# Optimization experiments

Hardware: AMD Instinct MI355X
Metric: run time of the kernel (lower is better)

The kernel has to match this reference:

```python
import jax, jax.numpy as jnp
import numpy as np

B, S, HID, NH, K = 4, 1500, 1024, 16, 64
DH = HID // NH  # 64


def _rel_bias(pos_emb, length):
    # pos_emb: [2K+1, d]; Shaw-style relative position embedding lookup -> [S, S, d]
    kk = (pos_emb.shape[0] - 1) // 2
    idx = jnp.arange(length)
    dist = jnp.clip(idx[None, :] - idx[:, None], -kk, kk) + kk
    return pos_emb[dist]


def setup_inputs() -> dict:
    key = jax.random.key(0)
    ks = jax.random.split(key, 12)
    sq = 1.0 / np.sqrt(HID)
    inp = {
        "query": jax.random.normal(ks[0], (B, S, HID), jnp.float32),
        "key": jax.random.normal(ks[1], (B, S, HID), jnp.float32),
        "value": jax.random.normal(ks[2], (B, S, HID), jnp.float32),
        # per-head QKV projections stacked over heads: [NH, HID, DH]
        "Wq": jax.random.normal(ks[3], (NH, HID, DH), jnp.float32) * sq,
        "bq": jnp.zeros((NH, DH), jnp.float32),
        "Wk": jax.random.normal(ks[4], (NH, HID, DH), jnp.float32) * sq,
        "bk": jnp.zeros((NH, DH), jnp.float32),
        "Wv": jax.random.normal(ks[5], (NH, HID, DH), jnp.float32) * sq,
        "bv": jnp.zeros((NH, DH), jnp.float32),
        # relative position tables [2K+1, DH]
        "pos_k": jax.random.normal(ks[6], (2 * K + 1, DH), jnp.float32) * 0.1,
        "pos_v": jax.random.normal(ks[7], (2 * K + 1, DH), jnp.float32) * 0.1,
        # output projection
        "W_fc": jax.random.normal(ks[8], (HID, HID), jnp.float32) * sq,
        "b_fc": jnp.zeros((HID,), jnp.float32),
    }
    return inp


def reference(query, key, value, Wq, bq, Wk, bk, Wv, bv, pos_k, pos_v, W_fc, b_fc):
    seq = query.shape[1]
    k_bias = _rel_bias(pos_k, seq)  # [S, S, DH]
    v_bias = _rel_bias(pos_v, seq)  # [S, S, DH]

    # batched per-head projections: [B, NH, S, DH]
    q = jnp.einsum('bsh,nhd->bnsd', query, Wq) + bq[None, :, None, :]
    k = jnp.einsum('bsh,nhd->bnsd', key, Wk) + bk[None, :, None, :]
    v = jnp.einsum('bsh,nhd->bnsd', value, Wv) + bv[None, :, None, :]

    attn_1 = jnp.einsum('bnqd,bnkd->bnqk', q, k)
    attn_2 = jnp.einsum('bnqd,qkd->bnqk', q, k_bias)  # Shaw relative key bias
    scores = (attn_1 + attn_2) / jnp.sqrt(jnp.float32(DH))
    w = jax.nn.softmax(scores, axis=-1)  # [B, NH, S, S]

    values_1 = jnp.einsum('bnqk,bnkd->bnqd', w, v)
    values_2 = jnp.einsum('bnqk,qkd->bnqd', w, v_bias)  # Shaw relative value bias
    heads = values_1 + values_2  # [B, NH, S, DH]

    # concat heads in head order -> [B, S, HID]
    hidden = jnp.transpose(heads, (0, 2, 1, 3)).reshape(query.shape[0], seq, -1)
    return hidden @ W_fc + b_fc
```

## Files before the change

kernel.cpp:

```cpp
#include <hip/hip_runtime.h>
#include <stdint.h>

typedef unsigned short u16;
typedef __attribute__((ext_vector_type(8))) short bf16x8;
typedef __attribute__((ext_vector_type(4))) float f32x4;

#define MFMA16(a, b, c) __builtin_amdgcn_mfma_f32_16x16x32_bf16(a, b, c, 0, 0, 0)

__device__ __forceinline__ u16 f2bf(float x) {
  union { float f; uint32_t u; } v; v.f = x;
  uint32_t r = (v.u + 0x7FFFu + ((v.u >> 16) & 1u)) >> 16;
  return (u16)r;
}
__device__ __forceinline__ float bf2f(u16 h) {
  union { uint32_t u; float f; } v; v.u = ((uint32_t)h) << 16; return v.f;
}
__device__ __forceinline__ uint cvt_pk_bf16(float a, float b) {
  uint r;
  asm("v_cvt_pk_bf16_f32 %0, %1, %2" : "=v"(r) : "v"(a), "v"(b));
  return r;
}
__device__ __forceinline__ void gll16(const void* g, void* s) {
  __builtin_amdgcn_global_load_lds((const __attribute__((address_space(1))) unsigned int*)g,
                                   (__attribute__((address_space(3))) unsigned int*)s, 16, 0, 0);
}


__global__ __launch_bounds__(256) void pack_x_kernel(const float* __restrict__ q,
                                                     const float* __restrict__ k,
                                                     const float* __restrict__ v,
                                                     u16* __restrict__ X) {
  const float* src = blockIdx.z == 0 ? q : (blockIdx.z == 1 ? k : v);
  u16* dst = X + (size_t)blockIdx.z * (6016UL * 1024UL);
  size_t idx = (size_t)blockIdx.x * 1024 + (size_t)threadIdx.x * 4;
  float4 f = *(const float4*)(src + idx);
  uint2 o;
  o.x = cvt_pk_bf16(f.x, f.y);
  o.y = cvt_pk_bf16(f.z, f.w);
  *(uint2*)(dst + idx) = o;
}

__global__ __launch_bounds__(256) void pack_w_kernel(const float* __restrict__ Wq,
                                                     const float* __restrict__ Wk,
                                                     const float* __restrict__ Wv,
                                                     const float* __restrict__ Wfc,
                                                     const float* __restrict__ bq,
                                                     const float* __restrict__ bk,
                                                     const float* __restrict__ bv,
                                                     const float* __restrict__ posk,
                                                     const float* __restrict__ posv,
                                                     u16* __restrict__ Wt,
                                                     u16* __restrict__ Wfct,
                                                     float* __restrict__ biascat,
                                                     u16* __restrict__ poskbf,
                                                     u16* __restrict__ posvT) {
  __shared__ float tile[64][65];
  const int bi = blockIdx.x;
  if (bi == 1024) {
    for (int i = threadIdx.x; i < 1024; i += 256) {
      biascat[i] = bq[i]; biascat[1024 + i] = bk[i]; biascat[2048 + i] = bv[i];
    }
    for (int i = threadIdx.x; i < 144 * 64; i += 256) {
      int r = i >> 6;
      poskbf[i] = (r < 129) ? f2bf(posk[i]) : (u16)0;
    }
    const int d = threadIdx.x & 63, rr = threadIdx.x >> 6;
#pragma unroll
    for (int j = 0; j < 34; ++j) {
      const int r = rr * 34 + j;
      posvT[d * 136 + r] = (r < 129) ? f2bf(posv[(size_t)r * 64 + d]) : (u16)0;
    }
    return;
  }
  const int r = threadIdx.x >> 2, c0 = (threadIdx.x & 3) * 16;
  const float* src;
  u16* outp;
  if (bi < 768) {
    const int z = bi >> 8, rem = bi & 255, n = rem >> 4, h0 = (rem & 15) * 64;
    const float* W = z == 0 ? Wq : (z == 1 ? Wk : Wv);
    src = W + (size_t)n * 65536 + (size_t)(h0 + r) * 64 + c0;
    outp = Wt + (size_t)z * (1024UL * 1024UL) + (size_t)(n * 64 + r) * 1024 + h0 + c0;
  } else {
    const int t = bi - 768;
    const int i0 = (t & 15) * 64, o0 = (t >> 4) * 64;
    src = Wfc + (size_t)(i0 + r) * 1024 + o0 + c0;
    outp = Wfct + (size_t)(o0 + r) * 1024 + i0 + c0;
  }
#pragma unroll
  for (int j = 0; j < 16; j += 4) {
    float4 f = *(const float4*)(src + j);
    tile[r][c0 + j] = f.x; tile[r][c0 + j + 1] = f.y;
    tile[r][c0 + j + 2] = f.z; tile[r][c0 + j + 3] = f.w;
  }
  __syncthreads();
#pragma unroll
  for (int j = 0; j < 16; ++j) outp[j] = f2bf(tile[c0 + j][r]);
}

__global__ __launch_bounds__(256) void vtrans_kernel(const u16* __restrict__ qkv,
                                                     u16* __restrict__ Vt) {
  const size_t ZS = 4UL * 16 * 1536 * 64;
  __shared__ u16 t[64][72];
  const int bh = blockIdx.x & 63, s0 = (blockIdx.x >> 6) * 64;
  const u16* src = qkv + 2 * ZS + (size_t)bh * (1536UL * 64UL) + (size_t)s0 * 64;
  const int r = threadIdx.x >> 2, c0 = (threadIdx.x & 3) * 16;
  *(uint4*)&t[r][c0]     = *(const uint4*)(src + (size_t)r * 64 + c0);
  *(uint4*)&t[r][c0 + 8] = *(const uint4*)(src + (size_t)r * 64 + c0 + 8);
  __syncthreads();
  uint4 a, bvec;
  uint tmp[8];
#pragma unroll
  for (int j = 0; j < 8; ++j)
    tmp[j] = (uint)t[c0 + 2 * j][r] | ((uint)t[c0 + 2 * j + 1][r] << 16);
  a.x = tmp[0]; a.y = tmp[1]; a.z = tmp[2]; a.w = tmp[3];
  bvec.x = tmp[4]; bvec.y = tmp[5]; bvec.z = tmp[6]; bvec.w = tmp[7];
  u16* dst = Vt + (size_t)(bh * 64 + r) * 1536 + s0 + c0;
  *(uint4*)dst = a;
  *(uint4*)(dst + 8) = bvec;
}

__global__ __launch_bounds__(256, 4) void gemm_bt_kernel(
    const u16* __restrict__ Abase, long aStride,
    const u16* __restrict__ Bbase, long bStride,
    const float* __restrict__ biasBase, long biasStride,
    u16* __restrict__ outBF, float* __restrict__ outF, int mode) {
  __shared__ u16 As[2][128 * 32];
  __shared__ u16 Bs[2][128 * 32];

  const int nwg = 376 * gridDim.z;
  const int cpx = nwg >> 3;
  const int lid = blockIdx.x + (blockIdx.y << 3) + blockIdx.z * 376;
  const int swz = (lid & 7) * cpx + (lid >> 3);
  const int z = swz / 376;
  const int rem = swz - z * 376;
  const int m0 = (rem >> 3) * 128, n0 = (rem & 7) * 128;

  const u16* A = Abase + (size_t)z * aStride;
  const u16* Bt = Bbase + (size_t)z * bStride;
  const float* bias = biasBase + (size_t)z * biasStride;
  const int tid = threadIdx.x, w = tid >> 6, lane = tid & 63;
  const int quad = lane >> 4, l16 = lane & 15;
  const int wm = w >> 1, wn = w & 1;
  const int srow = w * 16 + (lane >> 2);
  const int scol = (lane & 3) * 8;
  const u16* gA = A + (size_t)(m0 + srow) * 1024 + scol;
  const u16* gB = Bt + (size_t)(n0 + srow) * 1024 + scol;
  const int lo0 = (w * 16) * 32;
  const int lo1 = (64 + w * 16) * 32;

  f32x4 acc[4][4];
  const f32x4 zf = {0.f, 0.f, 0.f, 0.f};
#pragma unroll
  for (int a = 0; a < 4; ++a)
#pragma unroll
    for (int b = 0; b < 4; ++b) acc[a][b] = zf;

  auto stage = [&](int buf) {
    gll16(gA, &As[buf][lo0]);
    gll16(gA + 64 * 1024, &As[buf][lo1]);
    gll16(gB, &Bs[buf][lo0]);
    gll16(gB + 64 * 1024, &Bs[buf][lo1]);
    gA += 32; gB += 32;
  };
  auto compute = [&](int buf) {
    bf16x8 af[4], bfr[4];
#pragma unroll
    for (int f = 0; f < 4; ++f) {
      af[f]  = *(const bf16x8*)(&As[buf][(wm * 64 + f * 16 + l16) * 32 + quad * 8]);
      bfr[f] = *(const bf16x8*)(&Bs[buf][(wn * 64 + f * 16 + l16) * 32 + quad * 8]);
    }
#pragma unroll
    for (int fm = 0; fm < 4; ++fm)
#pragma unroll
      for (int fn = 0; fn < 4; ++fn)
        acc[fm][fn] = MFMA16(af[fm], bfr[fn], acc[fm][fn]);
  };

  stage(0);

#define GEMM_WAIT_BAR() do {                                  \
    asm volatile("s_waitcnt vmcnt(0)" ::: "memory");          \
    __builtin_amdgcn_sched_barrier(0);                        \
    __builtin_amdgcn_s_barrier();                             \
    __builtin_amdgcn_sched_barrier(0);                        \
  } while (0)

#pragma unroll 1
  for (int pr = 0; pr < 16; ++pr) {
    GEMM_WAIT_BAR();
    stage(1);
    compute(0);
    GEMM_WAIT_BAR();
    if (pr < 15) stage(0);
    compute(1);
  }
#undef GEMM_WAIT_BAR

  if (mode == 0) {
    const float scale = (z == 0) ? 0.125f : 1.0f;
    u16* out = outBF + (size_t)z * (4UL * 16 * 1536 * 64);
#pragma unroll
    for (int fm = 0; fm < 4; ++fm) {
#pragma unroll
      for (int i = 0; i < 4; ++i) {
        const int m = m0 + wm * 64 + fm * 16 + quad * 4 + i;
        if (m >= 6000) continue;
        const int bb = m / 1500;
        const int s = m - bb * 1500;
#pragma unroll
        for (int fn = 0; fn < 4; ++fn) {
          const int n = n0 + wn * 64 + fn * 16 + l16;
          const float vv = (acc[fm][fn][i] + bias[n]) * scale;
          const int h = n >> 6, d = n & 63;
          out[((size_t)(bb * 16 + h) * 1536 + s) * 64 + d] = f2bf(vv);
        }
      }
    }
  } else {
#pragma unroll
    for (int fm = 0; fm < 4; ++fm) {
#pragma unroll
      for (int i = 0; i < 4; ++i) {
        const int m = m0 + wm * 64 + fm * 16 + quad * 4 + i;
        if (m >= 6000) continue;
#pragma unroll
        for (int fn = 0; fn < 4; ++fn) {
          const int n = n0 + wn * 64 + fn * 16 + l16;
          outF[(size_t)m * 1024 + n] = acc[fm][fn][i] + bias[n];
        }
      }
    }
  }
}

__global__ __launch_bounds__(256, 4) void attn_kernel(const u16* __restrict__ qkv,
                                                      const u16* __restrict__ Vt,
                                                      const u16* __restrict__ poskbf,
                                                      const u16* __restrict__ posvT,
                                                      const float* __restrict__ posv,
                                                      u16* __restrict__ hidden) {
  const size_t ZS = 4UL * 16 * 1536 * 64;
  __shared__ u16 qb_s[64 * 136];
  __shared__ u16 kbuf[2][2048];
  __shared__ u16 vbuf[2][2048];

  const int tid = threadIdx.x;
  const int w = tid >> 6, lane = tid & 63, quad = lane >> 4, l16 = lane & 15;
  const int bi = blockIdx.x;
  const int bh = bi & 63;
  const int q0 = (bi >> 6) * 64, qw0 = q0 + w * 16;
  const int b = bh >> 4;
  const size_t sb = (size_t)bh * (1536UL * 64UL);
  const u16* Qp = qkv + sb;
  const u16* Kp = qkv + ZS + sb;
  const u16* Vtb = Vt + (size_t)bh * (64UL * 1536UL);
  u16* qb_row = qb_s + (w * 16 + l16) * 136;

  const int r8 = lane >> 3, c8 = lane & 7;
  const int vr = lane >> 2, vc = lane & 3;
  const int kprow = ((( (w * 8 + r8) & 15) >> 2) * 8) + (((w * 8 + r8) >> 4) * 4) + ((w * 8 + r8) & 3);
  const u16* kSrc = Kp + (size_t)kprow * 64 + ((c8 ^ r8) * 8);
  const u16* vSrc = Vtb + (size_t)(w * 16 + vr) * 1536 + ((vc ^ ((vr >> 1) & 3)) * 8);
  u16* const kDst = &kbuf[0][0] + w * 512;
  u16* const vDst = &vbuf[0][0] + w * 512;

  gll16(kSrc, kDst);
  gll16(vSrc, vDst);

  const u16* qptr = Qp + (size_t)(qw0 + l16) * 64 + quad * 8;
  const bf16x8 qB0 = *(const bf16x8*)qptr;
  const bf16x8 qB1 = *(const bf16x8*)(qptr + 32);

  const f32x4 zf = {0.f, 0.f, 0.f, 0.f};
#pragma unroll
  for (int nf = 0; nf < 9; ++nf) {
    const u16* bp = poskbf + (size_t)(nf * 16 + l16) * 64 + quad * 8;
    bf16x8 b0 = *(const bf16x8*)bp;
    bf16x8 b1 = *(const bf16x8*)(bp + 32);
    f32x4 c = zf;
    c = MFMA16(qB0, b0, c);
    c = MFMA16(qB1, b1, c);
    const int col = nf * 16 + l16;
    if (col < 136) {
#pragma unroll
      for (int i = 0; i < 4; ++i)
        qb_s[(w * 16 + quad * 4 + i) * 136 + col] = f2bf(c[i]);
    }
  }
  __syncthreads();

  const float L2E = 1.44269504f;
  const float M8 = -8.0f * L2E;
  const float eLow  = __builtin_fmaf(bf2f(qb_row[0]), L2E, M8);
  const float eHigh = __builtin_fmaf(bf2f(qb_row[128]), L2E, M8);

  f32x4 accf[4];
#pragma unroll
  for (int dc = 0; dc < 4; ++dc) accf[dc] = zf;
  float sSimple = 0.f, sLowSave = 0.f, sDall = 0.f, sD0 = 0.f, sD128 = 0.f;

  const int itLowEnd = (qw0 >= 95) ? (((qw0 - 95) >> 5) + 1) : 0;
  const int itHigh0 = (qw0 + 110) >> 5;
  const int dEnd = itHigh0 < 46 ? itHigh0 : 46;

  const int kswz = (quad ^ (l16 & 7)) * 8;
  const int kswz4 = ((quad + 4) ^ (l16 & 7)) * 8;
  const int vpos = (quad ^ ((l16 >> 1) & 3)) * 8;

  const u16* kS = kSrc + 2048;
  const u16* vS = vSrc + 32;

  auto body = [&](int it, const u16* kb, const u16* vbse, bool doStage, int stageOff) {
    if (doStage) {
      gll16(kS, kDst + stageOff);
      gll16(vS, vDst + stageOff);
      kS += 2048; vS += 32;
    }

    if (it == itLowEnd) sLowSave = sSimple;
    const int phase = (it < itLowEnd) ? 0 : ((it >= 46) ? 1 : ((it < dEnd) ? 1 : 2));

    bf16x8 ka00 = *(const bf16x8*)(kb + l16 * 64 + kswz);
    bf16x8 ka01 = *(const bf16x8*)(kb + l16 * 64 + kswz4);
    bf16x8 ka10 = *(const bf16x8*)(kb + (16 + l16) * 64 + kswz);
    bf16x8 ka11 = *(const bf16x8*)(kb + (16 + l16) * 64 + kswz4);
    bf16x8 vb0 = *(const bf16x8*)(vbse + l16 * 32 + vpos);
    bf16x8 vb1 = *(const bf16x8*)(vbse + (16 + l16) * 32 + vpos);
    bf16x8 vb2 = *(const bf16x8*)(vbse + (32 + l16) * 32 + vpos);
    bf16x8 vb3 = *(const bf16x8*)(vbse + (48 + l16) * 32 + vpos);

    float qb[2][4];
    if (phase == 1) {
      const int base = it * 32 + 64 - qw0 - l16 + quad * 8;
#pragma unroll
      for (int cg = 0; cg < 2; ++cg) {
#pragma unroll
        for (int i = 0; i < 4; ++i) {
          int delta = base + cg * 4 + i;
          delta = delta < 0 ? 0 : (delta > 128 ? 128 : delta);
          qb[cg][i] = bf2f(qb_row[delta]);
        }
      }
    }

    f32x4 cc[2];
    cc[0] = zf; cc[1] = zf;
    cc[0] = MFMA16(ka00, qB0, cc[0]);
    cc[0] = MFMA16(ka01, qB1, cc[0]);
    cc[1] = MFMA16(ka10, qB0, cc[1]);
    cc[1] = MFMA16(ka11, qB1, cc[1]);

    float pvv[2][4];
    if (phase != 1) {
      const float eB = (phase == 0) ? eLow : eHigh;
#pragma unroll
      for (int cg = 0; cg < 2; ++cg) {
#pragma unroll
        for (int i = 0; i < 4; ++i) {
          float p = __builtin_amdgcn_exp2f(__builtin_fmaf(cc[cg][i], L2E, eB));
          sSimple += p; pvv[cg][i] = p;
        }
      }
    } else {
      const int kc0 = it * 32;
#pragma unroll
      for (int cg = 0; cg < 2; ++cg) {
        const int krow0 = kc0 + quad * 8 + cg * 4;
        const int dbase = krow0 + 64 - qw0 - l16;
#pragma unroll
        for (int i = 0; i < 4; ++i) {
          int delta = dbase + i;
          delta = delta < 0 ? 0 : (delta > 128 ? 128 : delta);
          const float t = cc[cg][i] + qb[cg][i];
          float p = __builtin_amdgcn_exp2f(__builtin_fmaf(t, L2E, M8));
          if (krow0 + i >= 1500) p = 0.f;
          sDall += p;
          sD0   += (delta == 0)   ? p : 0.f;
          sD128 += (delta == 128) ? p : 0.f;
          pvv[cg][i] = p;
        }
        const uint pk01 = cvt_pk_bf16(pvv[cg][0], pvv[cg][1]);
        const uint pk23 = cvt_pk_bf16(pvv[cg][2], pvv[cg][3]);
        const u16 hb[4] = {(u16)pk01, (u16)(pk01 >> 16), (u16)pk23, (u16)(pk23 >> 16)};
#pragma unroll
        for (int i = 0; i < 4; ++i) {
          int delta = dbase + i;
          delta = delta < 0 ? 0 : (delta > 128 ? 128 : delta);
          if ((delta != 0) & (delta != 128)) qb_row[delta] = hb[i];
        }
      }
    }

    union { uint u[4]; bf16x8 v; } pa;
    pa.u[0] = cvt_pk_bf16(pvv[0][0], pvv[0][1]);
    pa.u[1] = cvt_pk_bf16(pvv[0][2], pvv[0][3]);
    pa.u[2] = cvt_pk_bf16(pvv[1][0], pvv[1][1]);
    pa.u[3] = cvt_pk_bf16(pvv[1][2], pvv[1][3]);

    accf[0] = MFMA16(pa.v, vb0, accf[0]);
    accf[1] = MFMA16(pa.v, vb1, accf[1]);
    accf[2] = MFMA16(pa.v, vb2, accf[2]);
    accf[3] = MFMA16(pa.v, vb3, accf[3]);

    __syncthreads();
  };

#pragma unroll 1
  for (int pr = 0; pr < 23; ++pr) {
    const int it0 = pr * 2;
    body(it0,     &kbuf[0][0], &vbuf[0][0], true, 2048);
    body(it0 + 1, &kbuf[1][0], &vbuf[1][0], true, 0);
  }
  body(46, &kbuf[0][0], &vbuf[0][0], false, 0);

  const float sLow = sLowSave;
  const float sHigh = sSimple - sLowSave;
  float lpart = sSimple + sDall;
  float clow = sLow + sD0;
  float chigh = sHigh + sD128;
#pragma unroll
  for (int m = 16; m <= 32; m <<= 1) {
    lpart += __shfl_xor(lpart, m);
    clow  += __shfl_xor(clow, m);
    chigh += __shfl_xor(chigh, m);
  }
  const float linv = 1.0f / lpart;

  {
    const int qg_row = qw0 + l16;
    if (quad == 0) qb_row[0] = 0;
    const int lim = 64 - qg_row;
    for (int d = 1 + quad; d < lim; d += 4) qb_row[d] = 0;
    const int dlo = 1564 - qg_row;
    for (int d = dlo + quad; d <= 127; d += 4) qb_row[d] = 0;
  }

  f32x4 o2[4];
#pragma unroll
  for (int dc = 0; dc < 4; ++dc) o2[dc] = zf;
#pragma unroll
  for (int kk = 0; kk < 4; ++kk) {
    bf16x8 pa2 = *(const bf16x8*)(qb_row + kk * 32 + quad * 8);
#pragma unroll
    for (int dc = 0; dc < 4; ++dc) {
      bf16x8 vb2r = *(const bf16x8*)(posvT + (size_t)(dc * 16 + l16) * 136 + kk * 32 + quad * 8);
      o2[dc] = MFMA16(pa2, vb2r, o2[dc]);
    }
  }

  float li[4], cl[4], ch[4];
#pragma unroll
  for (int i = 0; i < 4; ++i) {
    const int srcl = quad * 4 + i;
    li[i] = __shfl(linv, srcl);
    cl[i] = __shfl(clow, srcl);
    ch[i] = __shfl(chigh, srcl);
  }

#pragma unroll
  for (int dc = 0; dc < 4; ++dc) {
    const int d = dc * 16 + l16;
    const float pv0 = posv[d], pv1 = posv[128 * 64 + d];
#pragma unroll
    for (int i = 0; i < 4; ++i) {
      const int qg = qw0 + quad * 4 + i;
      if (qg < 1500) {
        const float val = (accf[dc][i] + o2[dc][i] + cl[i] * pv0 + ch[i] * pv1) * li[i];
        hidden[((size_t)(b * 1500 + qg)) * 1024 + (bh & 15) * 64 + d] = f2bf(val);
      }
    }
  }
}

extern "C" void kernel_launch(void* const* d_in, const int* in_sizes, int n_in,
                              void* d_out, int out_size, void* d_ws, size_t ws_size,
                              hipStream_t stream) {
  const float* query = (const float*)d_in[0];
  const float* key   = (const float*)d_in[1];
  const float* value = (const float*)d_in[2];
  const float* Wq = (const float*)d_in[3];
  const float* bq = (const float*)d_in[4];
  const float* Wk = (const float*)d_in[5];
  const float* bk = (const float*)d_in[6];
  const float* Wv = (const float*)d_in[7];
  const float* bv = (const float*)d_in[8];
  const float* posk = (const float*)d_in[9];
  const float* posv = (const float*)d_in[10];
  const float* Wfc = (const float*)d_in[11];
  const float* bfc = (const float*)d_in[12];
  float* out = (float*)d_out;

  char* p = (char*)d_ws;
  u16* X = (u16*)p;        p += 3UL * 6016 * 1024 * 2;
  u16* Wt = (u16*)p;       p += 3UL * 1024 * 1024 * 2;
  u16* Wfct = (u16*)p;     p += 1024UL * 1024 * 2;
  u16* poskbf = (u16*)p;   p += 144UL * 64 * 2;
  u16* posvT = (u16*)p;    p += 64UL * 136 * 2;
  float* biascat = (float*)p; p += 3UL * 1024 * 4;
  u16* qkv = (u16*)p;      p += 3UL * 4 * 16 * 1536 * 64 * 2;
  u16* hidden = X;
  u16* Vt = X + 6291456;

  pack_x_kernel<<<dim3(6000, 1, 3), 256, 0, stream>>>(query, key, value, X);
  pack_w_kernel<<<dim3(1025), 256, 0, stream>>>(Wq, Wk, Wv, Wfc, bq, bk, bv, posk, posv,
                                                Wt, Wfct, biascat, poskbf, posvT);

  gemm_bt_kernel<<<dim3(8, 47, 3), 256, 0, stream>>>(
      X, 6016L * 1024, Wt, 1024L * 1024, biascat, 1024L, qkv, nullptr, 0);

  vtrans_kernel<<<dim3(1536), 256, 0, stream>>>(qkv, Vt);

  attn_kernel<<<dim3(1536), 256, 0, stream>>>(qkv, Vt, poskbf, posvT, posv, hidden);

  gemm_bt_kernel<<<dim3(8, 47, 1), 256, 0, stream>>>(
      hidden, 0L, Wfct, 0L, bfc, 0L, nullptr, out, 1);
}
```

Before: 354.0 us.

## Fuse input bf16 conversion and V transpose into QKV projection GEMM

The QKV GEMM now reads fp32 activations directly, converts them to bf16 in registers and writes them to LDS, replacing the separate pack kernel. The V-projection epilogue transposes through shared memory and writes Vt directly, removing the vtrans kernel. This eliminates two kernel launches and a full round trip of bf16 activations through global memory. The cost is that A-tile loads pass through registers instead of async global-to-LDS loads, which may lengthen the GEMM main loop.

New measurement: 348.4 us. Within noise of the previous version (-1.6%).

```diff
diff --git a/kernel.cpp b/kernel.cpp
--- a/kernel.cpp
+++ b/kernel.cpp
@@ -25,20 +25,6 @@
                                    (__attribute__((address_space(3))) unsigned int*)s, 16, 0, 0);
 }
 
-
-__global__ __launch_bounds__(256) void pack_x_kernel(const float* __restrict__ q,
-                                                     const float* __restrict__ k,
-                                                     const float* __restrict__ v,
-                                                     u16* __restrict__ X) {
-  const float* src = blockIdx.z == 0 ? q : (blockIdx.z == 1 ? k : v);
-  u16* dst = X + (size_t)blockIdx.z * (6016UL * 1024UL);
-  size_t idx = (size_t)blockIdx.x * 1024 + (size_t)threadIdx.x * 4;
-  float4 f = *(const float4*)(src + idx);
-  uint2 o;
-  o.x = cvt_pk_bf16(f.x, f.y);
-  o.y = cvt_pk_bf16(f.z, f.w);
-  *(uint2*)(dst + idx) = o;
-}
 
 __global__ __launch_bounds__(256) void pack_w_kernel(const float* __restrict__ Wq,
                                                      const float* __restrict__ Wk,
@@ -97,35 +83,13 @@
   for (int j = 0; j < 16; ++j) outp[j] = f2bf(tile[c0 + j][r]);
 }
 
-__global__ __launch_bounds__(256) void vtrans_kernel(const u16* __restrict__ qkv,
-                                                     u16* __restrict__ Vt) {
-  const size_t ZS = 4UL * 16 * 1536 * 64;
-  __shared__ u16 t[64][72];
-  const int bh = blockIdx.x & 63, s0 = (blockIdx.x >> 6) * 64;
-  const u16* src = qkv + 2 * ZS + (size_t)bh * (1536UL * 64UL) + (size_t)s0 * 64;
-  const int r = threadIdx.x >> 2, c0 = (threadIdx.x & 3) * 16;
-  *(uint4*)&t[r][c0]     = *(const uint4*)(src + (size_t)r * 64 + c0);
-  *(uint4*)&t[r][c0 + 8] = *(const uint4*)(src + (size_t)r * 64 + c0 + 8);
-  __syncthreads();
-  uint4 a, bvec;
-  uint tmp[8];
-#pragma unroll
-  for (int j = 0; j < 8; ++j)
-    tmp[j] = (uint)t[c0 + 2 * j][r] | ((uint)t[c0 + 2 * j + 1][r] << 16);
-  a.x = tmp[0]; a.y = tmp[1]; a.z = tmp[2]; a.w = tmp[3];
-  bvec.x = tmp[4]; bvec.y = tmp[5]; bvec.z = tmp[6]; bvec.w = tmp[7];
-  u16* dst = Vt + (size_t)(bh * 64 + r) * 1536 + s0 + c0;
-  *(uint4*)dst = a;
-  *(uint4*)(dst + 8) = bvec;
-}
-
 __global__ __launch_bounds__(256, 4) void gemm_bt_kernel(
-    const u16* __restrict__ Abase, long aStride,
+    const float* __restrict__ aQ, const float* __restrict__ aK, const float* __restrict__ aV,
+    const u16* __restrict__ Ahid,
     const u16* __restrict__ Bbase, long bStride,
     const float* __restrict__ biasBase, long biasStride,
-    u16* __restrict__ outBF, float* __restrict__ outF, int mode) {
-  __shared__ u16 As[2][128 * 32];
-  __shared__ u16 Bs[2][128 * 32];
+    u16* __restrict__ outBF, u16* __restrict__ VtOut, float* __restrict__ outF, int mode) {
+  __shared__ u16 smem[17408];
 
   const int nwg = 376 * gridDim.z;
   const int cpx = nwg >> 3;
@@ -135,7 +99,6 @@
   const int rem = swz - z * 376;
   const int m0 = (rem >> 3) * 128, n0 = (rem & 7) * 128;
 
-  const u16* A = Abase + (size_t)z * aStride;
   const u16* Bt = Bbase + (size_t)z * bStride;
   const float* bias = biasBase + (size_t)z * biasStride;
   const int tid = threadIdx.x, w = tid >> 6, lane = tid & 63;
@@ -143,10 +106,10 @@
   const int wm = w >> 1, wn = w & 1;
   const int srow = w * 16 + (lane >> 2);
   const int scol = (lane & 3) * 8;
-  const u16* gA = A + (size_t)(m0 + srow) * 1024 + scol;
-  const u16* gB = Bt + (size_t)(n0 + srow) * 1024 + scol;
-  const int lo0 = (w * 16) * 32;
-  const int lo1 = (64 + w * 16) * 32;
+
+  const u16* gB0 = Bt + (size_t)(n0 + srow) * 1024 + scol;
+  const u16* gB1 = gB0 + 64UL * 1024;
+  const int slab = (w * 16) * 32;
 
   f32x4 acc[4][4];
   const f32x4 zf = {0.f, 0.f, 0.f, 0.f};
@@ -155,19 +118,17 @@
 #pragma unroll
     for (int b = 0; b < 4; ++b) acc[a][b] = zf;
 
-  auto stage = [&](int buf) {
-    gll16(gA, &As[buf][lo0]);
-    gll16(gA + 64 * 1024, &As[buf][lo1]);
-    gll16(gB, &Bs[buf][lo0]);
-    gll16(gB + 64 * 1024, &Bs[buf][lo1]);
-    gA += 32; gB += 32;
+  auto gllB = [&](int buf) {
+    gll16(gB0, &smem[8192 + buf * 4096 + slab]);
+    gll16(gB1, &smem[8192 + buf * 4096 + slab + 64 * 32]);
+    gB0 += 32; gB1 += 32;
   };
   auto compute = [&](int buf) {
     bf16x8 af[4], bfr[4];
 #pragma unroll
     for (int f = 0; f < 4; ++f) {
-      af[f]  = *(const bf16x8*)(&As[buf][(wm * 64 + f * 16 + l16) * 32 + quad * 8]);
-      bfr[f] = *(const bf16x8*)(&Bs[buf][(wn * 64 + f * 16 + l16) * 32 + quad * 8]);
+      af[f]  = *(const bf16x8*)&smem[buf * 4096 + (wm * 64 + f * 16 + l16) * 32 + quad * 8];
+      bfr[f] = *(const bf16x8*)&smem[8192 + buf * 4096 + (wn * 64 + f * 16 + l16) * 32 + quad * 8];
     }
 #pragma unroll
     for (int fm = 0; fm < 4; ++fm)
@@ -176,47 +137,144 @@
         acc[fm][fn] = MFMA16(af[fm], bfr[fn], acc[fm][fn]);
   };
 
-  stage(0);
-
-#define GEMM_WAIT_BAR() do {                                  \
-    asm volatile("s_waitcnt vmcnt(0)" ::: "memory");          \
-    __builtin_amdgcn_sched_barrier(0);                        \
-    __builtin_amdgcn_s_barrier();                             \
-    __builtin_amdgcn_sched_barrier(0);                        \
-  } while (0)
+  if (mode == 0) {
+    const float* srcF = z == 0 ? aQ : (z == 1 ? aK : aV);
+    int rowA0 = m0 + srow;        if (rowA0 > 5999) rowA0 = 5999;
+    int rowA1 = m0 + 64 + srow;   if (rowA1 > 5999) rowA1 = 5999;
+    const float* fA0 = srcF + (size_t)rowA0 * 1024 + scol;
+    const float* fA1 = srcF + (size_t)rowA1 * 1024 + scol;
+    float4 a00, a01, a10, a11;
+    auto loadA = [&]() {
+      a00 = *(const float4*)fA0; a01 = *(const float4*)(fA0 + 4);
+      a10 = *(const float4*)fA1; a11 = *(const float4*)(fA1 + 4);
+      fA0 += 32; fA1 += 32;
+    };
+    const int adst = (w * 16 + (lane >> 2)) * 32 + (lane & 3) * 8;
+    auto dswriteA = [&](int buf) {
+      uint4 lo, hi;
+      lo.x = cvt_pk_bf16(a00.x, a00.y); lo.y = cvt_pk_bf16(a00.z, a00.w);
+      lo.z = cvt_pk_bf16(a01.x, a01.y); lo.w = cvt_pk_bf16(a01.z, a01.w);
+      hi.x = cvt_pk_bf16(a10.x, a10.y); hi.y = cvt_pk_bf16(a10.z, a10.w);
+      hi.z = cvt_pk_bf16(a11.x, a11.y); hi.w = cvt_pk_bf16(a11.z, a11.w);
+      *(uint4*)&smem[buf * 4096 + adst] = lo;
+      *(uint4*)&smem[buf * 4096 + adst + 64 * 32] = hi;
+    };
+
+    loadA();
+    gllB(0);
+
+#define QKV_SYNC(BUF) do {                                    \
+      asm volatile("s_waitcnt vmcnt(0)" ::: "memory");        \
+      __builtin_amdgcn_sched_barrier(0);                      \
+      dswriteA(BUF);                                          \
+      asm volatile("s_waitcnt lgkmcnt(0)" ::: "memory");      \
+      __builtin_amdgcn_sched_barrier(0);                      \
+      __builtin_amdgcn_s_barrier();                           \
+      __builtin_amdgcn_sched_barrier(0);                      \
+    } while (0)
 
 #pragma unroll 1
-  for (int pr = 0; pr < 16; ++pr) {
-    GEMM_WAIT_BAR();
-    stage(1);
-    compute(0);
-    GEMM_WAIT_BAR();
-    if (pr < 15) stage(0);
-    compute(1);
-  }
-#undef GEMM_WAIT_BAR
-
-  if (mode == 0) {
-    const float scale = (z == 0) ? 0.125f : 1.0f;
-    u16* out = outBF + (size_t)z * (4UL * 16 * 1536 * 64);
-#pragma unroll
-    for (int fm = 0; fm < 4; ++fm) {
-#pragma unroll
-      for (int i = 0; i < 4; ++i) {
-        const int m = m0 + wm * 64 + fm * 16 + quad * 4 + i;
-        if (m >= 6000) continue;
-        const int bb = m / 1500;
-        const int s = m - bb * 1500;
+    for (int pr = 0; pr < 16; ++pr) {
+      QKV_SYNC(0);
+      loadA(); gllB(1);
+      compute(0);
+      QKV_SYNC(1);
+      if (pr < 15) { loadA(); gllB(0); }
+      compute(1);
+    }
+#undef QKV_SYNC
+
+    if (z < 2) {
+      const float scale = (z == 0) ? 0.125f : 1.0f;
+      u16* out = outBF + (size_t)z * (4UL * 16 * 1536 * 64);
+#pragma unroll
+      for (int fm = 0; fm < 4; ++fm) {
+#pragma unroll
+        for (int i = 0; i < 4; ++i) {
+          const int m = m0 + wm * 64 + fm * 16 + quad * 4 + i;
+          if (m >= 6000) continue;
+          const int bb = m / 1500;
+          const int s = m - bb * 1500;
+#pragma unroll
+          for (int fn = 0; fn < 4; ++fn) {
+            const int n = n0 + wn * 64 + fn * 16 + l16;
+            const float vv = (acc[fm][fn][i] + bias[n]) * scale;
+            const int h = n >> 6, d = n & 63;
+            out[((size_t)(bb * 16 + h) * 1536 + s) * 64 + d] = f2bf(vv);
+          }
+        }
+      }
+    } else {
+      __syncthreads();
+      u16* T = smem;
+#pragma unroll
+      for (int fm = 0; fm < 4; ++fm) {
+        const int ml = wm * 64 + fm * 16 + quad * 4;
 #pragma unroll
         for (int fn = 0; fn < 4; ++fn) {
-          const int n = n0 + wn * 64 + fn * 16 + l16;
-          const float vv = (acc[fm][fn][i] + bias[n]) * scale;
-          const int h = n >> 6, d = n & 63;
-          out[((size_t)(bb * 16 + h) * 1536 + s) * 64 + d] = f2bf(vv);
+          const int nl = wn * 64 + fn * 16 + l16;
+          const float b0 = bias[n0 + nl];
+          uint2 pk;
+          pk.x = cvt_pk_bf16(acc[fm][fn][0] + b0, acc[fm][fn][1] + b0);
+          pk.y = cvt_pk_bf16(acc[fm][fn][2] + b0, acc[fm][fn][3] + b0);
+          *(uint2*)&T[nl * 136 + ml] = pk;
+        }
+      }
+      __syncthreads();
+#pragma unroll 1
+      for (int ps = 0; ps < 8; ++ps) {
+        const int row = ps * 16 + (tid >> 4);
+        const int col = (tid & 15) * 8;
+        const int ng = n0 + row;
+        const int h = ng >> 6, d = ng & 63;
+        const int mg = m0 + col;
+        uint4 v = *(const uint4*)&T[row * 136 + col];
+        const int bb0 = mg / 1500, bb7 = (mg + 7) / 1500;
+        if ((bb0 == bb7) & (mg + 7 < 6000)) {
+          u16* dst = VtOut + ((size_t)((bb0 * 16 + h) * 64 + d)) * 1536 + (mg - bb0 * 1500);
+          uint2 loh; loh.x = v.x; loh.y = v.y;
+          uint2 hih; hih.x = v.z; hih.y = v.w;
+          *(uint2*)dst = loh;
+          *(uint2*)(dst + 4) = hih;
+        } else {
+          const u16* tv = (const u16*)&v;
+#pragma unroll
+          for (int j = 0; j < 8; ++j) {
+            const int m = mg + j;
+            if (m < 6000) {
+              const int bb = m / 1500;
+              VtOut[((size_t)((bb * 16 + h) * 64 + d)) * 1536 + (m - bb * 1500)] = tv[j];
+            }
+          }
         }
       }
     }
   } else {
+    const u16* gA0 = Ahid + (size_t)(m0 + srow) * 1024 + scol;
+    const u16* gA1 = gA0 + 64UL * 1024;
+    auto stage1 = [&](int buf) {
+      gll16(gA0, &smem[buf * 4096 + slab]);
+      gll16(gA1, &smem[buf * 4096 + slab + 64 * 32]);
+      gA0 += 32; gA1 += 32;
+      gllB(buf);
+    };
+    stage1(0);
+#define FC_SYNC() do {                                        \
+      asm volatile("s_waitcnt vmcnt(0)" ::: "memory");        \
+      __builtin_amdgcn_sched_barrier(0);                      \
+      __builtin_amdgcn_s_barrier();                           \
+      __builtin_amdgcn_sched_barrier(0);                      \
+    } while (0)
+#pragma unroll 1
+    for (int pr = 0; pr < 16; ++pr) {
+      FC_SYNC();
+      stage1(1);
+      compute(0);
+      FC_SYNC();
+      if (pr < 15) stage1(0);
+      compute(1);
+    }
+#undef FC_SYNC
 #pragma unroll
     for (int fm = 0; fm < 4; ++fm) {
 #pragma unroll
@@ -501,17 +559,14 @@
   u16* hidden = X;
   u16* Vt = X + 6291456;
 
-  pack_x_kernel<<<dim3(6000, 1, 3), 256, 0, stream>>>(query, key, value, X);
   pack_w_kernel<<<dim3(1025), 256, 0, stream>>>(Wq, Wk, Wv, Wfc, bq, bk, bv, posk, posv,
                                                 Wt, Wfct, biascat, poskbf, posvT);
 
   gemm_bt_kernel<<<dim3(8, 47, 3), 256, 0, stream>>>(
-      X, 6016L * 1024, Wt, 1024L * 1024, biascat, 1024L, qkv, nullptr, 0);
-
-  vtrans_kernel<<<dim3(1536), 256, 0, stream>>>(qkv, Vt);
+      query, key, value, nullptr, Wt, 1024L * 1024, biascat, 1024L, qkv, Vt, nullptr, 0);
 
   attn_kernel<<<dim3(1536), 256, 0, stream>>>(qkv, Vt, poskbf, posvT, posv, hidden);
 
   gemm_bt_kernel<<<dim3(8, 47, 1), 256, 0, stream>>>(
-      hidden, 0L, Wfct, 0L, bfc, 0L, nullptr, out, 1);
-}
+      nullptr, nullptr, nullptr, hidden, Wfct, 0L, bfc, 0L, nullptr, nullptr, out, 1);
+}
```
